# Performance work log

Measured on AMD Instinct MI355X. Metric: run time of the kernel, lower is better.

Reference implementation:

```python
import jax, jax.numpy as jnp
import numpy as np

HID = 64      # hidden_dim
HEADS = 4     # attention heads
CH = HID // HEADS  # 16 per-head channels
EDIM = 6      # edge_dim
NEG = 0.2     # leaky_relu negative slope


def _glorot(key, shape):
    fan_in, fan_out = shape[0], shape[-1]
    s = np.sqrt(6.0 / (fan_in + fan_out)).astype(np.float32)
    return jax.random.uniform(key, shape, jnp.float32, -s, s)


def setup_inputs() -> dict:
    key = jax.random.key(0)
    ks = iter(jax.random.split(key, 48))
    N, E, T = 100000, 1200000, 20000
    inp = {
        "x": jax.random.normal(next(ks), (N, 7), jnp.float32),
        "pos": jax.random.normal(next(ks), (N, 3), jnp.float32),
        "node_type": jax.random.randint(next(ks), (N,), 0, 2),
        "edge_index": jax.random.randint(next(ks), (2, E), 0, N),
        "edge_attr": jax.random.normal(next(ks), (E, EDIM), jnp.float32),
        "num_tracks": T,
        "hidden_state": jax.random.normal(next(ks), (T, HID), jnp.float32),
        # params
        "type_emb": jax.random.normal(next(ks), (2, 8), jnp.float32),
        "enc_W1": _glorot(next(ks), (18, HID)), "enc_b1": jnp.zeros((HID,), jnp.float32),
        "enc_W2": _glorot(next(ks), (HID, HID)), "enc_b2": jnp.zeros((HID,), jnp.float32),
        "gru_Wi": _glorot(next(ks), (HID, 3 * HID)), "gru_bi": jnp.zeros((3 * HID,), jnp.float32),
        "gru_Wh": _glorot(next(ks), (HID, 3 * HID)), "gru_bh": jnp.zeros((3 * HID,), jnp.float32),
        "dec_W1": _glorot(next(ks), (HID, HID)), "dec_b1": jnp.zeros((HID,), jnp.float32),
        "dec_W2": _glorot(next(ks), (HID, 7)), "dec_b2": jnp.zeros((7,), jnp.float32),
    }
    for g in ("g1", "g2"):
        inp[g + "_Wl"] = _glorot(next(ks), (HID, HID))
        inp[g + "_bl"] = jnp.zeros((HID,), jnp.float32)
        inp[g + "_Wr"] = _glorot(next(ks), (HID, HID))
        inp[g + "_br"] = jnp.zeros((HID,), jnp.float32)
        inp[g + "_We"] = _glorot(next(ks), (EDIM, HID))
        inp[g + "_att"] = _glorot(next(ks), (HEADS, CH))
        inp[g + "_bias"] = jnp.zeros((HID,), jnp.float32)
    return inp


def _segment_softmax(e, seg, n):
    m = jax.ops.segment_max(e, seg, num_segments=n)
    m = jnp.where(jnp.isfinite(m), m, 0.0)
    ex = jnp.exp(e - m[seg])
    s = jax.ops.segment_sum(ex, seg, num_segments=n)
    return ex / (s[seg] + 1e-16)


def _gatv2(h, src, dst, eattr, Wl, bl, Wr, br, We, att, bias):
    N = h.shape[0]
    xl = (h @ Wl + bl).reshape(N, HEADS, CH)
    xr = (h @ Wr + br).reshape(N, HEADS, CH)
    ea = (eattr @ We).reshape(-1, HEADS, CH)
    g = jax.nn.leaky_relu(xl[src] + xr[dst] + ea, NEG)      # [E, H, C]
    e = jnp.einsum('ehc,hc->eh', g, att)                     # [E, H]
    alpha = _segment_softmax(e, dst, N)                      # [E, H]
    msg = xl[src] * alpha[..., None]                         # [E, H, C]
    out = jax.ops.segment_sum(msg, dst, num_segments=N)
    return out.reshape(N, HID) + bias, alpha


def reference(x, pos, node_type, edge_index, edge_attr, num_tracks, hidden_state,
              type_emb, enc_W1, enc_b1, enc_W2, enc_b2,
              g1_Wl, g1_bl, g1_Wr, g1_br, g1_We, g1_att, g1_bias,
              g2_Wl, g2_bl, g2_Wr, g2_br, g2_We, g2_att, g2_bias,
              gru_Wi, gru_bi, gru_Wh, gru_bh,
              dec_W1, dec_b1, dec_W2, dec_b2):
    N = x.shape[0]
    h = jnp.concatenate([x, pos, type_emb[node_type]], axis=-1)
    h = jax.nn.relu(h @ enc_W1 + enc_b1) @ enc_W2 + enc_b2

    # PyG GATv2Conv: add self loops, edge_attr fill_value='mean' (mean of incoming edges)
    src, dst = edge_index[0], edge_index[1]
    deg = jax.ops.segment_sum(jnp.ones(src.shape[0], jnp.float32), dst, num_segments=N)
    loop_attr = jax.ops.segment_sum(edge_attr, dst, num_segments=N) / jnp.maximum(deg, 1.0)[:, None]
    ar = jnp.arange(N)
    src_a = jnp.concatenate([src, ar])
    dst_a = jnp.concatenate([dst, ar])
    eattr_a = jnp.concatenate([edge_attr, loop_attr], axis=0)

    h1, a1 = _gatv2(h, src_a, dst_a, eattr_a, g1_Wl, g1_bl, g1_Wr, g1_br, g1_We, g1_att, g1_bias)
    h1 = jax.nn.relu(h1)
    h2, a2 = _gatv2(h1, src_a, dst_a, eattr_a, g2_Wl, g2_bl, g2_Wr, g2_br, g2_We, g2_att, g2_bias)

    # GRUCell on the first num_tracks nodes
    ht = h2[:num_tracks]
    gi = ht @ gru_Wi + gru_bi
    gh = hidden_state @ gru_Wh + gru_bh
    r = jax.nn.sigmoid(gi[:, :HID] + gh[:, :HID])
    z = jax.nn.sigmoid(gi[:, HID:2 * HID] + gh[:, HID:2 * HID])
    n = jnp.tanh(gi[:, 2 * HID:] + r * gh[:, 2 * HID:])
    new_tracks = (1.0 - z) * n + z * hidden_state

    new_full = jnp.concatenate([new_tracks, h2[num_tracks:]], axis=0)
    out = jax.nn.relu(new_full @ dec_W1 + dec_b1) @ dec_W2 + dec_b2  # [N, 7]
    final = out.at[:, :3].set(pos + out[:, :3])
    final = final.at[:, 3:6].set(x[:, :3] + out[:, 3:6])
    return final, new_full, a1, a2
```

## Files before the change

### kernel.cpp

```cpp
#include <hip/hip_runtime.h>

#define NEG 0.2f
#define LOG2E 1.44269504088896f
typedef unsigned short u16;

__device__ __forceinline__ float sigmoidf_(float v){ return 1.f/(1.f+__expf(-v)); }
__device__ __forceinline__ int rfl_(int v){ return __builtin_amdgcn_readfirstlane(v); }
__device__ __forceinline__ float bf2f_(unsigned u){ return __uint_as_float(u<<16); }
__device__ __forceinline__ u16 f2bf_(float f){
  unsigned u = __float_as_uint(f);
  u += 0x7FFFu + ((u>>16)&1u);
  return (u16)(u>>16);
}
template<int C>
__device__ __forceinline__ float dppadd_(float p){
  int r = __builtin_amdgcn_update_dpp(0, __float_as_int(p), C, 0xF, 0xF, true);
  return p + __int_as_float(r);
}
__device__ __forceinline__ float dppsum16_(float p){
  p = dppadd_<0x121>(p);
  p = dppadd_<0x122>(p);
  p = dppadd_<0x124>(p);
  p = dppadd_<0x128>(p);
  return p;
}

__global__ void deg_kernel(const int* __restrict__ ei, int* __restrict__ deg, int E)
{
  int base = blockIdx.x*1024 + threadIdx.x;
  #pragma unroll
  for (int j=0;j<4;j++){
    int e = base + j*256;
    if (e < E) atomicAdd(deg + ei[E+e], 1);
  }
}

__global__ __launch_bounds__(256) void alloc_kernel(
    const int* __restrict__ deg, int* __restrict__ offs, int* __restrict__ cursor,
    int* __restrict__ counter, int N)
{
  __shared__ int wsum[4], woff[4], sbase;
  int lane = threadIdx.x & 63, w = threadIdx.x >> 6;
  int base = blockIdx.x*1024 + threadIdx.x*4;
  int v[4]; int s=0;
  #pragma unroll
  for (int j=0;j<4;j++){ int i=base+j; v[j]=(i<N)?deg[i]:0; s+=v[j]; }
  int inc=s;
  #pragma unroll
  for (int d=1;d<64;d<<=1){ int t=__shfl_up(inc,d); if (lane>=d) inc+=t; }
  if (lane==63) wsum[w]=inc;
  __syncthreads();
  if (threadIdx.x==0){
    woff[0]=0; woff[1]=wsum[0]; woff[2]=wsum[0]+wsum[1]; woff[3]=wsum[0]+wsum[1]+wsum[2];
    sbase = atomicAdd(counter, woff[3]+wsum[3]);
  }
  __syncthreads();
  int excl = sbase + woff[w] + (inc - s);
  #pragma unroll
  for (int j=0;j<4;j++){
    int i=base+j;
    if (i<N){ offs[i]=excl; cursor[i]=excl; }
    excl+=v[j];
  }
}

__global__ __launch_bounds__(256) void encxfill_kernel(
    const float* __restrict__ x, const float* __restrict__ pos,
    const int* __restrict__ ntype, const float* __restrict__ temb,
    const float* __restrict__ eW1, const float* __restrict__ eb1,
    const float* __restrict__ eW2, const float* __restrict__ eb2,
    const float* __restrict__ Wl, const float* __restrict__ bl,
    const float* __restrict__ Wr, const float* __restrict__ br,
    u16* __restrict__ xlo, u16* __restrict__ xro,
    const int* __restrict__ ei, const float* __restrict__ eattr,
    int* __restrict__ cursor, float4* __restrict__ slots,
    int exB, int E, int N)
{
  __shared__ float fT[4][8*20];
  __shared__ float tT[4][8*64];
  if ((int)blockIdx.x >= exB){
    int base = ((int)blockIdx.x - exB)*1024 + (int)threadIdx.x;
    #pragma unroll
    for (int j=0;j<4;j++){
      int e = base + j*256;
      if (e < E){
        int dst = ei[E + e];
        unsigned slot = (unsigned)atomicAdd(cursor + dst, 1);
        const float2* ep = (const float2*)(eattr + (size_t)e*6);
        float2 p0=ep[0], p1=ep[1], p2=ep[2];
        float4 a, b;
        a.x = __int_as_float(e); a.y = __int_as_float(ei[e]);
        a.z = p0.x; a.w = p0.y;
        b.x = p1.x; b.y = p1.y; b.z = p2.x; b.w = p2.y;
        slots[slot*2u]   = a;
        slots[slot*2u+1] = b;
      }
    }
    return;
  }
  int lane = threadIdx.x & 63;
  int wid  = threadIdx.x >> 6;
  int n0 = (blockIdx.x*4 + wid)*8;
  if (n0 >= N) return;
  #pragma unroll
  for (int m=0;m<8;m++){
    int n=n0+m; float fv=0.f;
    if (n<N){
      if (lane<7)       fv=x[(size_t)n*7+lane];
      else if (lane<10) fv=pos[(size_t)n*3+lane-7];
      else if (lane<18) fv=temb[ntype[n]*8+lane-10];
    }
    if (lane<20) fT[wid][m*20+lane]=fv;
  }
  float t[8];
  float b1v=eb1[lane];
  #pragma unroll
  for (int m=0;m<8;m++) t[m]=b1v;
  #pragma unroll 2
  for (int k=0;k<18;k++){
    float w=eW1[k*64+lane];
    #pragma unroll
    for (int m=0;m<8;m++) t[m] += fT[wid][m*20+k]*w;
  }
  #pragma unroll
  for (int m=0;m<8;m++){ t[m]=fmaxf(t[m],0.f); tT[wid][m*64+lane]=t[m]; }
  float o[8];
  float b2v=eb2[lane];
  #pragma unroll
  for (int m=0;m<8;m++) o[m]=b2v;
  #pragma unroll 2
  for (int k=0;k<64;k++){
    float w=eW2[k*64+lane];
    #pragma unroll
    for (int m=0;m<8;m++) o[m] += tT[wid][m*64+k]*w;
  }
  #pragma unroll
  for (int m=0;m<8;m++) tT[wid][m*64+lane]=o[m];
  float blv=bl[lane], brv=br[lane];
  float al[8], ar[8];
  #pragma unroll
  for (int m=0;m<8;m++){ al[m]=blv; ar[m]=brv; }
  #pragma unroll 2
  for (int k=0;k<64;k++){
    float wl=Wl[k*64+lane], wr=Wr[k*64+lane];
    #pragma unroll
    for (int m=0;m<8;m++){
      float hb = tT[wid][m*64+k];
      al[m]+=hb*wl; ar[m]+=hb*wr;
    }
  }
  #pragma unroll
  for (int m=0;m<8;m++){
    int n=n0+m;
    if (n<N){ xlo[(((unsigned)n)<<6)+lane]=f2bf_(al[m]); xro[(((unsigned)n)<<6)+lane]=f2bf_(ar[m]); }
  }
}

__global__ __launch_bounds__(256) void xfrm_kernel(
    const float* __restrict__ hin,
    const float* __restrict__ Wl, const float* __restrict__ bl,
    const float* __restrict__ Wr, const float* __restrict__ br,
    u16* __restrict__ xlo, u16* __restrict__ xro, int N)
{
  __shared__ float sWl[4096], sWr[4096];
  __shared__ float hT[4][16*64];
  for (int i=threadIdx.x;i<4096;i+=256){ sWl[i]=Wl[i]; sWr[i]=Wr[i]; }
  __syncthreads();
  int lane=threadIdx.x&63;
  int wid=threadIdx.x>>6;
  int n0=(blockIdx.x*4+wid)*16;
  if (n0>=N) return;
  #pragma unroll
  for (int m=0;m<16;m++){
    int n=n0+m;
    hT[wid][m*64+lane] = (n<N)? hin[(size_t)n*64+lane] : 0.f;
  }
  float blv=bl[lane], brv=br[lane];
  float al[16], ar[16];
  #pragma unroll
  for (int m=0;m<16;m++){ al[m]=blv; ar[m]=brv; }
  #pragma unroll 2
  for (int k=0;k<64;k++){
    float wl=sWl[k*64+lane], wr=sWr[k*64+lane];
    #pragma unroll
    for (int m=0;m<16;m++){
      float hb = hT[wid][m*64+k];
      al[m]+=hb*wl; ar[m]+=hb*wr;
    }
  }
  #pragma unroll
  for (int m=0;m<16;m++){
    int n=n0+m;
    if (n<N){ xlo[(((unsigned)n)<<6)+lane]=f2bf_(al[m]); xro[(((unsigned)n)<<6)+lane]=f2bf_(ar[m]); }
  }
}

#define EDGE_STEP(EIDX, EADD, XV) do {                                       \
    float s_ = (XV) + xrv + (EADD);                                          \
    s_ = fmaxf(s_, NEG*s_);                                                  \
    float p_ = dppsum16_(s_*attv);                                           \
    if (isbase) aout[(((unsigned)(EIDX))<<2)+h] = p_;                        \
    if (__all(p_ <= mmax)) {                                                 \
      float w_ = exp2f(p_ - mmax);                                           \
      ssum += w_; acc += w_*(XV);                                            \
    } else {                                                                 \
      float mn_ = fmaxf(mmax, p_);                                           \
      float sc_ = exp2f(mmax - mn_);                                         \
      float w_  = exp2f(p_ - mn_);                                           \
      ssum = ssum*sc_ + w_;                                                  \
      acc  = acc*sc_ + w_*(XV);                                              \
      mmax = mn_;                                                            \
    }                                                                        \
  } while(0)

#define EDGE_PRE(J, OO) \
    float4 u##J = slots[(unsigned)(OO)*2u], v##J = slots[(unsigned)(OO)*2u+1u]; \
    int e##J = rfl_(__float_as_int(u##J.x)); \
    int s##J = rfl_(__float_as_int(u##J.y)); \
    unsigned xv##J = xlb[(((unsigned)s##J)<<6)+lane];

#define EDGE_BODY(J) \
    float d##J = u##J.z*we0 + u##J.w*we1 + v##J.x*we2 + v##J.y*we3 + v##J.z*we4 + v##J.w*we5; \
    dsum += d##J; \
    EDGE_STEP(e##J, d##J, bf2f_(xv##J));

__global__ __launch_bounds__(256) void gat_kernel(
    const float4* __restrict__ slots, const int* __restrict__ offs, const int* __restrict__ deg,
    const u16* __restrict__ xlb, const u16* __restrict__ xrb,
    const float* __restrict__ We, const float* __restrict__ att,
    const float* __restrict__ bias,
    float* __restrict__ aout, float2* __restrict__ msbuf,
    float* __restrict__ hout,
    int E, int N, int do_relu)
{
  int lane = threadIdx.x & 63;
  int n = blockIdx.x*4 + (threadIdx.x>>6);
  if (n >= N) return;
  float we0=We[lane], we1=We[64+lane], we2=We[128+lane],
        we3=We[192+lane], we4=We[256+lane], we5=We[320+lane];
  float attv = att[lane] * LOG2E;
  float bv = bias[lane];
  float xrv = bf2f_(xrb[(((unsigned)n)<<6)+lane]);
  int h = lane >> 4;
  bool isbase = (lane & 15) == 0;
  int o0 = rfl_(offs[n]);
  int dg = rfl_(deg[n]);
  int oend = o0 + dg;
  float mmax = -3.402823e38f, ssum=0.f, acc=0.f, dsum=0.f;
  int o = o0;
  for (; o+4 <= oend; o += 4){
    EDGE_PRE(0,o); EDGE_PRE(1,o+1); EDGE_PRE(2,o+2); EDGE_PRE(3,o+3);
    EDGE_BODY(0); EDGE_BODY(1); EDGE_BODY(2); EDGE_BODY(3);
  }
  for (; o < oend; ++o){
    EDGE_PRE(0,o);
    EDGE_BODY(0);
  }
  {
    float dS = dsum * (1.f/fmaxf((float)dg,1.f));
    float xvS = bf2f_((unsigned)xlb[(((unsigned)n)<<6)+lane]);
    EDGE_STEP(E+n, dS, xvS);
  }
  float sinv = 1.f/(ssum + 1e-16f);
  if (isbase) msbuf[(((unsigned)n)<<2)+h] = make_float2(mmax, sinv);
  float outv = acc*sinv + bv;
  if (do_relu) outv = fmaxf(outv, 0.f);
  hout[(((unsigned)n)<<6)+lane] = outv;
}

__global__ void alpha_kernel(const int* __restrict__ ei,
                             const float2* __restrict__ ms1, const float2* __restrict__ ms2,
                             float4* __restrict__ a1, float4* __restrict__ a2, int E, int N)
{
  int e = blockIdx.x*256 + threadIdx.x;
  if (e >= E+N) return;
  int dst = (e<E)? ei[E+e] : (e-E);
  {
    float4 r = a1[e];
    const float2* mp = ms1 + (((unsigned)dst)<<2);
    float2 m0=mp[0], m1=mp[1], m2=mp[2], m3=mp[3];
    float4 o;
    o.x = exp2f(r.x - m0.x)*m0.y;
    o.y = exp2f(r.y - m1.x)*m1.y;
    o.z = exp2f(r.z - m2.x)*m2.y;
    o.w = exp2f(r.w - m3.x)*m3.y;
    a1[e] = o;
  }
  {
    float4 r = a2[e];
    const float2* mp = ms2 + (((unsigned)dst)<<2);
    float2 m0=mp[0], m1=mp[1], m2=mp[2], m3=mp[3];
    float4 o;
    o.x = exp2f(r.x - m0.x)*m0.y;
    o.y = exp2f(r.y - m1.x)*m1.y;
    o.z = exp2f(r.z - m2.x)*m2.y;
    o.w = exp2f(r.w - m3.x)*m3.y;
    a2[e] = o;
  }
}

__global__ __launch_bounds__(256) void grudec_kernel(
    const float* __restrict__ h2, const float* __restrict__ hid,
    const float* __restrict__ Wi, const float* __restrict__ bi,
    const float* __restrict__ Wh, const float* __restrict__ bh,
    const int* __restrict__ Tptr,
    const float* __restrict__ W1, const float* __restrict__ b1,
    const float* __restrict__ W2, const float* __restrict__ b2,
    const float* __restrict__ x, const float* __restrict__ pos,
    float* __restrict__ nf, float* __restrict__ fout, int N)
{
  __shared__ float sW2[448];
  __shared__ float sb2[8];
  __shared__ float tT[4][8*68];
  __shared__ float pT[4][8*68];
  for (int i=threadIdx.x;i<448;i+=256) sW2[i]=W2[i];
  if (threadIdx.x<7)  sb2[threadIdx.x]=b2[threadIdx.x];
  __syncthreads();
  int lane = threadIdx.x & 63;
  int wid  = threadIdx.x >> 6;
  int n0 = (blockIdx.x*4 + wid)*8;
  if (n0 >= N) return;
  int T = *Tptr;
  float hv[8], nfv[8];
  #pragma unroll
  for (int m=0;m<8;m++){ int n=n0+m; hv[m] = (n<N)? h2[(size_t)n*64+lane] : 0.f; }
  if (n0 < T){
    float pv[8];
    #pragma unroll
    for (int m=0;m<8;m++){ int n=n0+m; pv[m] = (n<T)? hid[(size_t)n*64+lane] : 0.f; }
    #pragma unroll
    for (int m=0;m<8;m++){ tT[wid][m*68+lane]=hv[m]; pT[wid][m*68+lane]=pv[m]; }
    float gr[8],gz[8],gn[8],hr[8],hz[8],hn[8];
    #pragma unroll
    for (int m=0;m<8;m++){ gr[m]=0.f;gz[m]=0.f;gn[m]=0.f;hr[m]=0.f;hz[m]=0.f;hn[m]=0.f; }
    for (int k=0;k<64;k++){
      float wir=Wi[k*192+lane], wiz=Wi[k*192+64+lane], win=Wi[k*192+128+lane];
      float whr=Wh[k*192+lane], whz=Wh[k*192+64+lane], whn=Wh[k*192+128+lane];
      #pragma unroll
      for (int m=0;m<8;m++){
        float a=tT[wid][m*68+k], b=pT[wid][m*68+k];
        gr[m]+=a*wir; gz[m]+=a*wiz; gn[m]+=a*win;
        hr[m]+=b*whr; hz[m]+=b*whz; hn[m]+=b*whn;
      }
    }
    float bir=bi[lane], biz=bi[64+lane], bin=bi[128+lane];
    float bhr=bh[lane], bhz=bh[64+lane], bhn=bh[128+lane];
    #pragma unroll
    for (int m=0;m<8;m++){
      int n=n0+m;
      if (n<T){
        float r  = sigmoidf_(gr[m]+bir + hr[m]+bhr);
        float z  = sigmoidf_(gz[m]+biz + hz[m]+bhz);
        float nn = tanhf(gn[m]+bin + r*(hn[m]+bhn));
        nfv[m] = (1.f-z)*nn + z*pv[m];
      } else {
        nfv[m] = hv[m];
      }
    }
  } else {
    #pragma unroll
    for (int m=0;m<8;m++) nfv[m] = hv[m];
  }
  #pragma unroll
  for (int m=0;m<8;m++){ int n=n0+m; if (n<N) nf[(size_t)n*64+lane]=nfv[m]; }
  #pragma unroll
  for (int m=0;m<8;m++) tT[wid][m*68+lane]=nfv[m];
  float t[8];
  float b1v=b1[lane];
  #pragma unroll
  for (int m=0;m<8;m++) t[m]=b1v;
  #pragma unroll 2
  for (int k=0;k<64;k++){
    float w=W1[k*64+lane];
    #pragma unroll
    for (int m=0;m<8;m++) t[m] += tT[wid][m*68+k]*w;
  }
  #pragma unroll
  for (int m=0;m<8;m++) t[m]=fmaxf(t[m],0.f);
  #pragma unroll
  for (int m=0;m<8;m++) tT[wid][m*68+lane]=t[m];
  int mm = lane >> 3, cc = lane & 7;
  if (cc < 7){
    float a2v = sb2[cc];
    #pragma unroll 4
    for (int k=0;k<64;k++) a2v += tT[wid][mm*68+k]*sW2[k*7+cc];
    int n = n0+mm;
    if (n < N){
      if (cc<3)      a2v += pos[(size_t)n*3+cc];
      else if (cc<6) a2v += x[(size_t)n*7+(cc-3)];
      fout[(size_t)n*7+cc] = a2v;
    }
  }
}

extern "C" void kernel_launch(void* const* d_in, const int* in_sizes, int n_in,
                              void* d_out, int out_size, void* d_ws, size_t ws_size,
                              hipStream_t stream)
{
  const float* x     = (const float*)d_in[0];
  const float* pos   = (const float*)d_in[1];
  const int*   ntype = (const int*)d_in[2];
  const int*   eidx  = (const int*)d_in[3];
  const float* eattr = (const float*)d_in[4];
  const int*   Tptr  = (const int*)d_in[5];
  const float* hid   = (const float*)d_in[6];
  const float* temb  = (const float*)d_in[7];
  const float* encW1 = (const float*)d_in[8];
  const float* encb1 = (const float*)d_in[9];
  const float* encW2 = (const float*)d_in[10];
  const float* encb2 = (const float*)d_in[11];
  const float* gruWi = (const float*)d_in[12];
  const float* grubi = (const float*)d_in[13];
  const float* gruWh = (const float*)d_in[14];
  const float* grubh = (const float*)d_in[15];
  const float* decW1 = (const float*)d_in[16];
  const float* decb1 = (const float*)d_in[17];
  const float* decW2 = (const float*)d_in[18];
  const float* decb2 = (const float*)d_in[19];
  const float* gWl[2]  = {(const float*)d_in[20], (const float*)d_in[27]};
  const float* gbl[2]  = {(const float*)d_in[21], (const float*)d_in[28]};
  const float* gWr[2]  = {(const float*)d_in[22], (const float*)d_in[29]};
  const float* gbr[2]  = {(const float*)d_in[23], (const float*)d_in[30]};
  const float* gWe[2]  = {(const float*)d_in[24], (const float*)d_in[31]};
  const float* gatt[2] = {(const float*)d_in[25], (const float*)d_in[32]};
  const float* gbias[2]= {(const float*)d_in[26], (const float*)d_in[33]};

  int N  = in_sizes[0] / 7;
  int E  = in_sizes[3] / 2;
  int Ea = E + N;

  char* w = (char*)d_ws;
  float* A      = (float*)w; w += (size_t)N*64*sizeof(float);
  u16*   XL     = (u16*)w;  w += (size_t)N*64*sizeof(u16);
  u16*   XR     = (u16*)w;  w += (size_t)N*64*sizeof(u16);
  float2* msbuf1= (float2*)w; w += (size_t)N*4*sizeof(float2);
  float2* msbuf2= (float2*)w; w += (size_t)N*4*sizeof(float2);
  float4* slots = (float4*)w; w += (size_t)E*32;
  int*   deg    = (int*)w;   w += (size_t)N*sizeof(int);
  int*   counter= (int*)w;   w += 4*sizeof(int);
  int*   cursor = (int*)w;   w += (size_t)N*sizeof(int);
  int*   offs   = (int*)w;   w += (size_t)N*sizeof(int);

  float* out_final = (float*)d_out;
  float* out_nf    = out_final + (size_t)N*7;
  float* out_a1    = out_nf + (size_t)N*64;
  float* out_a2    = out_a1 + (size_t)Ea*4;

  hipMemsetAsync(deg, 0, ((size_t)N + 4)*sizeof(int), stream);

  deg_kernel<<<(E+1023)/1024, 256, 0, stream>>>(eidx, deg, E);
  alloc_kernel<<<(N+1023)/1024, 256, 0, stream>>>(deg, offs, cursor, counter, N);

  int exB = (N+31)/32;
  int flB = (E+1023)/1024;
  encxfill_kernel<<<exB+flB, 256, 0, stream>>>(x, pos, ntype, temb,
      encW1, encb1, encW2, encb2, gWl[0], gbl[0], gWr[0], gbr[0], XL, XR,
      eidx, eattr, cursor, slots, exB, E, N);

  int gatB = (N+3)/4;
  gat_kernel<<<gatB, 256, 0, stream>>>(slots, offs, deg, XL, XR,
      gWe[0], gatt[0], gbias[0], out_a1, msbuf1, A, E, N, 1);

  int xfB = (N+63)/64;
  xfrm_kernel<<<xfB, 256, 0, stream>>>(A, gWl[1], gbl[1], gWr[1], gbr[1], XL, XR, N);

  gat_kernel<<<gatB, 256, 0, stream>>>(slots, offs, deg, XL, XR,
      gWe[1], gatt[1], gbias[1], out_a2, msbuf2, A, E, N, 0);

  grudec_kernel<<<(N+31)/32, 256, 0, stream>>>(A, hid, gruWi, grubi, gruWh, grubh, Tptr,
      decW1, decb1, decW2, decb2, x, pos, out_nf, out_final, N);

  alpha_kernel<<<(Ea+255)/256, 256, 0, stream>>>(eidx, msbuf1, msbuf2,
      (float4*)out_a1, (float4*)out_a2, E, N);
}
```

Measured before the change: 495.3 us.

## Split alpha normalization and fuse halves into second GAT and GRU/decoder launches

The standalone alpha normalization kernel is split into its layer-1 and layer-2 halves. The layer-1 half runs as extra blocks inside the second GAT launch, since it only depends on layer-1 results. The layer-2 half runs as extra blocks inside the GRU/decoder launch. This removes one launch and lets the memory-bound alpha rewrite overlap with independent compute, at the cost of heterogeneous blocks and shared memory being reserved in the grudec launch even for alpha blocks.

```diff
diff --git a/kernel.cpp b/kernel.cpp
--- a/kernel.cpp
+++ b/kernel.cpp
@@ -23,6 +23,22 @@
   p = dppadd_<0x124>(p);
   p = dppadd_<0x128>(p);
   return p;
+}
+
+__device__ __forceinline__ void alpha_body_(int e, const int* __restrict__ ei,
+    const float2* __restrict__ ms, float4* __restrict__ a, int E, int N)
+{
+  if (e >= E+N) return;
+  int dst = (e<E)? ei[E+e] : (e-E);
+  float4 r = a[e];
+  const float2* mp = ms + (((unsigned)dst)<<2);
+  float2 m0=mp[0], m1=mp[1], m2=mp[2], m3=mp[3];
+  float4 o;
+  o.x = exp2f(r.x - m0.x)*m0.y;
+  o.y = exp2f(r.y - m1.x)*m1.y;
+  o.z = exp2f(r.z - m2.x)*m2.y;
+  o.w = exp2f(r.w - m3.x)*m3.y;
+  a[e] = o;
 }
 
 __global__ void deg_kernel(const int* __restrict__ ei, int* __restrict__ deg, int E)
@@ -224,17 +240,15 @@
     dsum += d##J; \
     EDGE_STEP(e##J, d##J, bf2f_(xv##J));
 
-__global__ __launch_bounds__(256) void gat_kernel(
+__device__ __forceinline__ void gat_node_(int n,
     const float4* __restrict__ slots, const int* __restrict__ offs, const int* __restrict__ deg,
     const u16* __restrict__ xlb, const u16* __restrict__ xrb,
     const float* __restrict__ We, const float* __restrict__ att,
     const float* __restrict__ bias,
     float* __restrict__ aout, float2* __restrict__ msbuf,
-    float* __restrict__ hout,
-    int E, int N, int do_relu)
+    float* __restrict__ hout, int E, int N, int do_relu)
 {
   int lane = threadIdx.x & 63;
-  int n = blockIdx.x*4 + (threadIdx.x>>6);
   if (n >= N) return;
   float we0=We[lane], we1=We[64+lane], we2=We[128+lane],
         we3=We[192+lane], we4=We[256+lane], we5=We[320+lane];
@@ -268,38 +282,39 @@
   hout[(((unsigned)n)<<6)+lane] = outv;
 }
 
-__global__ void alpha_kernel(const int* __restrict__ ei,
-                             const float2* __restrict__ ms1, const float2* __restrict__ ms2,
-                             float4* __restrict__ a1, float4* __restrict__ a2, int E, int N)
-{
-  int e = blockIdx.x*256 + threadIdx.x;
-  if (e >= E+N) return;
-  int dst = (e<E)? ei[E+e] : (e-E);
-  {
-    float4 r = a1[e];
-    const float2* mp = ms1 + (((unsigned)dst)<<2);
-    float2 m0=mp[0], m1=mp[1], m2=mp[2], m3=mp[3];
-    float4 o;
-    o.x = exp2f(r.x - m0.x)*m0.y;
-    o.y = exp2f(r.y - m1.x)*m1.y;
-    o.z = exp2f(r.z - m2.x)*m2.y;
-    o.w = exp2f(r.w - m3.x)*m3.y;
-    a1[e] = o;
-  }
-  {
-    float4 r = a2[e];
-    const float2* mp = ms2 + (((unsigned)dst)<<2);
-    float2 m0=mp[0], m1=mp[1], m2=mp[2], m3=mp[3];
-    float4 o;
-    o.x = exp2f(r.x - m0.x)*m0.y;
-    o.y = exp2f(r.y - m1.x)*m1.y;
-    o.z = exp2f(r.z - m2.x)*m2.y;
-    o.w = exp2f(r.w - m3.x)*m3.y;
-    a2[e] = o;
-  }
-}
-
-__global__ __launch_bounds__(256) void grudec_kernel(
+__global__ __launch_bounds__(256) void gat_kernel(
+    const float4* __restrict__ slots, const int* __restrict__ offs, const int* __restrict__ deg,
+    const u16* __restrict__ xlb, const u16* __restrict__ xrb,
+    const float* __restrict__ We, const float* __restrict__ att,
+    const float* __restrict__ bias,
+    float* __restrict__ aout, float2* __restrict__ msbuf,
+    float* __restrict__ hout,
+    int E, int N, int do_relu)
+{
+  int n = blockIdx.x*4 + (threadIdx.x>>6);
+  gat_node_(n, slots, offs, deg, xlb, xrb, We, att, bias, aout, msbuf, hout, E, N, do_relu);
+}
+
+__global__ __launch_bounds__(256) void gat2alpha_kernel(
+    const float4* __restrict__ slots, const int* __restrict__ offs, const int* __restrict__ deg,
+    const u16* __restrict__ xlb, const u16* __restrict__ xrb,
+    const float* __restrict__ We, const float* __restrict__ att,
+    const float* __restrict__ bias,
+    float* __restrict__ aout, float2* __restrict__ msbuf,
+    float* __restrict__ hout,
+    const int* __restrict__ ei, const float2* __restrict__ ms1, float4* __restrict__ a1,
+    int alB, int E, int N, int do_relu)
+{
+  int idx = blockIdx.x;
+  if (idx < alB){
+    alpha_body_(idx*256 + (int)threadIdx.x, ei, ms1, a1, E, N);
+    return;
+  }
+  int n = (idx - alB)*4 + (threadIdx.x>>6);
+  gat_node_(n, slots, offs, deg, xlb, xrb, We, att, bias, aout, msbuf, hout, E, N, do_relu);
+}
+
+__global__ __launch_bounds__(256) void grudecalpha_kernel(
     const float* __restrict__ h2, const float* __restrict__ hid,
     const float* __restrict__ Wi, const float* __restrict__ bi,
     const float* __restrict__ Wh, const float* __restrict__ bh,
@@ -307,12 +322,20 @@
     const float* __restrict__ W1, const float* __restrict__ b1,
     const float* __restrict__ W2, const float* __restrict__ b2,
     const float* __restrict__ x, const float* __restrict__ pos,
-    float* __restrict__ nf, float* __restrict__ fout, int N)
+    float* __restrict__ nf, float* __restrict__ fout,
+    const int* __restrict__ ei,
+    const float2* __restrict__ ms2, float4* __restrict__ a2,
+    int gdB, int E, int N)
 {
   __shared__ float sW2[448];
   __shared__ float sb2[8];
   __shared__ float tT[4][8*68];
   __shared__ float pT[4][8*68];
+  if ((int)blockIdx.x >= gdB){
+    int e = ((int)blockIdx.x - gdB)*256 + (int)threadIdx.x;
+    alpha_body_(e, ei, ms2, a2, E, N);
+    return;
+  }
   for (int i=threadIdx.x;i<448;i+=256) sW2[i]=W2[i];
   if (threadIdx.x<7)  sb2[threadIdx.x]=b2[threadIdx.x];
   __syncthreads();
@@ -464,12 +487,13 @@
   int xfB = (N+63)/64;
   xfrm_kernel<<<xfB, 256, 0, stream>>>(A, gWl[1], gbl[1], gWr[1], gbr[1], XL, XR, N);
 
-  gat_kernel<<<gatB, 256, 0, stream>>>(slots, offs, deg, XL, XR,
-      gWe[1], gatt[1], gbias[1], out_a2, msbuf2, A, E, N, 0);
-
-  grudec_kernel<<<(N+31)/32, 256, 0, stream>>>(A, hid, gruWi, grubi, gruWh, grubh, Tptr,
-      decW1, decb1, decW2, decb2, x, pos, out_nf, out_final, N);
-
-  alpha_kernel<<<(Ea+255)/256, 256, 0, stream>>>(eidx, msbuf1, msbuf2,
-      (float4*)out_a1, (float4*)out_a2, E, N);
-}
+  int alB = (Ea+255)/256;
+  gat2alpha_kernel<<<alB+gatB, 256, 0, stream>>>(slots, offs, deg, XL, XR,
+      gWe[1], gatt[1], gbias[1], out_a2, msbuf2, A,
+      eidx, msbuf1, (float4*)out_a1, alB, E, N, 0);
+
+  int gdB = (N+31)/32;
+  grudecalpha_kernel<<<gdB+alB, 256, 0, stream>>>(A, hid, gruWi, grubi, gruWh, grubh, Tptr,
+      decW1, decb1, decW2, decb2, x, pos, out_nf, out_final,
+      eidx, msbuf2, (float4*)out_a2, gdB, E, N);
+}
```

Result: faster. 480.4 us (median of 2 runs) (-3.0%).
